# Optimization experiments

Hardware: AMD Instinct MI355X
Metric: run time of the kernel (lower is better)

Reference implementation:

```python
import jax, jax.numpy as jnp
import numpy as np

E = 256  # embedding_dim

def setup_inputs() -> dict:
    key = jax.random.key(0)
    k1, k2, k3 = jax.random.split(key, 3)
    B, P, N, D = 32, 4, 1024, E
    x = jax.random.normal(k1, (B, P, N, D), dtype=jnp.float32)
    W_qkv = jax.random.normal(k2, (D, 1 + 2 * E), dtype=jnp.float32) * (1.0 / np.sqrt(D))
    b_qkv = jnp.zeros((1 + 2 * E,), dtype=jnp.float32)
    W_o = jax.random.normal(k3, (E, E), dtype=jnp.float32) * (1.0 / np.sqrt(E))
    b_o = jnp.zeros((E,), dtype=jnp.float32)
    return {"x": x, "W_qkv": W_qkv, "b_qkv": b_qkv, "W_o": W_o, "b_o": b_o}

def reference(x, W_qkv, b_qkv, W_o, b_o):
    # qkv projection: [B,P,N,D] @ [D,1+2E] -> [B,P,N,1+2E]
    qkv = jnp.einsum('bpnd,de->bpne', x, W_qkv) + b_qkv
    q = qkv[..., :1]                 # [B,P,N,1]
    k = qkv[..., 1:1 + E]            # [B,P,N,E]
    v = jax.nn.relu(qkv[..., 1 + E:])  # [B,P,N,E]
    # softmax over patch axis N (axis=2)
    context_scores = jax.nn.softmax(q, axis=2)
    # context vector: sum over N of k * scores -> [B,P,1,E]
    context_vector = jnp.sum(k * context_scores, axis=2, keepdims=True)
    # broadcast-multiply with relu(v): [B,P,N,E] * [B,P,1,E]
    updated_values = v * context_vector
    # output projection
    out = jnp.einsum('bpnd,de->bpne', updated_values, W_o) + b_o
    return out
```

## Files before the change

### kernel.cpp

```cpp
#include <hip/hip_runtime.h>
#include <hip/hip_bf16.h>

typedef float f32x4 __attribute__((ext_vector_type(4)));
typedef short s16x8 __attribute__((ext_vector_type(8)));
typedef __bf16 bf16x8 __attribute__((ext_vector_type(8)));
typedef unsigned short u16;

#define NSEQ 1024
#define EDIM 256

#define WAITVM(N) asm volatile("s_waitcnt vmcnt(" #N ")" ::: "memory")

__device__ __forceinline__ u16 f2bf(float f){
  union { float f; unsigned u; } v; v.f = f;
  unsigned r = v.u + 0x7FFF + ((v.u >> 16) & 1);
  return (u16)(r >> 16);
}
__device__ __forceinline__ float bf2f(u16 b){
  union { float f; unsigned u; } v; v.u = ((unsigned)b) << 16;
  return v.f;
}

template <typename V>
__device__ __forceinline__ auto mfma_impl(V a, V b, f32x4 c, int)
    -> decltype(__builtin_amdgcn_mfma_f32_16x16x32_bf16(a, b, c, 0, 0, 0)) {
  return __builtin_amdgcn_mfma_f32_16x16x32_bf16(a, b, c, 0, 0, 0);
}
template <typename V>
__device__ __forceinline__ f32x4 mfma_impl(V a, V b, f32x4 c, long){
  bf16x8 ab = __builtin_bit_cast(bf16x8, a);
  bf16x8 bb = __builtin_bit_cast(bf16x8, b);
  return __builtin_amdgcn_mfma_f32_16x16x32_bf16(ab, bb, c, 0, 0, 0);
}
__device__ __forceinline__ f32x4 mfma16(s16x8 a, s16x8 b, f32x4 c){
  return mfma_impl(a, b, c, 0);
}

__device__ __forceinline__ void gload_lds16(const u16* g, u16* l){
  __builtin_amdgcn_global_load_lds((const __attribute__((address_space(1))) void*)g,
                                   (__attribute__((address_space(3))) void*)l, 16, 0, 0);
}

__global__ void k0_prep(const float* __restrict__ Wqkv, const float* __restrict__ Wo,
                        u16* __restrict__ wvf, u16* __restrict__ wof, float* __restrict__ wqc){
  int t = blockIdx.x * 256 + threadIdx.x;
  if (t < 16384){
    int which = t >> 13;
    int slot  = t & 8191;
    int l  = slot & 63;
    int nt = (slot >> 6) & 1;
    int ks = (slot >> 7) & 7;
    int c  = (slot >> 10) & 7;
    int row = ks*32 + 8*(l>>4);
    int col = c*32 + nt*16 + (l&15);
    s16x8 o8;
    if (which == 0){
      for (int j=0;j<8;j++) o8[j] = (short)f2bf(Wqkv[(size_t)(row+j)*513 + 257 + col]);
      *(s16x8*)(wvf + (size_t)slot*8) = o8;
    } else {
      for (int j=0;j<8;j++) o8[j] = (short)f2bf(Wo[(size_t)(row+j)*256 + col]);
      *(s16x8*)(wof + (size_t)slot*8) = o8;
    }
  } else if (t < 16384 + 256){
    int d = t - 16384;
    wqc[d] = Wqkv[(size_t)d*513];
  }
}

__global__ void k1_qfrag(const float* __restrict__ x, const float* __restrict__ wqc,
                         const float* __restrict__ bqkv, u16* __restrict__ xf, float* __restrict__ q){
  int bp = blockIdx.x >> 6, rt = blockIdx.x & 63;
  const float* xt = x + ((size_t)bp*NSEQ + rt*16) * EDIM;
  __shared__ float xl[16][260];
  int tid = threadIdx.x;
  for (int i=0;i<4;i++){
    int idx = tid + i*256;
    float4 vv = ((const float4*)xt)[idx];
    int row = idx >> 6, c4 = idx & 63;
    *(float4*)&xl[row][c4*4] = vv;
  }
  __syncthreads();
  int l = tid & 63, w = tid >> 6;
  int lo = l & 15, hi = l >> 4;
  for (int kk=0;kk<2;kk++){
    int ks = w*2 + kk;
    int k0 = ks*32 + 8*hi;
    s16x8 o8;
    for (int j=0;j<8;j++) o8[j] = (short)f2bf(xl[lo][k0+j]);
    size_t fo = ((((size_t)bp*64 + rt)*8 + ks)*64 + l) * 8;
    *(s16x8*)(xf + fo) = o8;
  }
  int c = l*4;
  float4 wv4 = *(const float4*)(wqc + c);
  float b0 = bqkv[0];
  for (int r=0;r<4;r++){
    int row = w*4 + r;
    float4 xv = *(float4*)&xl[row][c];
    float p = xv.x*wv4.x + xv.y*wv4.y + xv.z*wv4.z + xv.w*wv4.w;
    for (int o=32;o;o>>=1) p += __shfl_down(p, o);
    if (l == 0) q[(size_t)bp*NSEQ + rt*16 + row] = p + b0;
  }
}

__global__ __launch_bounds__(512) void k234(
    const u16* __restrict__ xf, const float* __restrict__ q,
    const float* __restrict__ Wqkv, const float* __restrict__ bqkv,
    float* __restrict__ cv){
  int bp = blockIdx.x;
  int tid = threadIdx.x, l = tid & 63, w = tid >> 6;
  int lo = l & 15, hi = l >> 4;
  __shared__ float sm[1024];
  __shared__ float red[16];
  __shared__ float tl[256];
  __shared__ float cvp[2][256];

  float2 v = ((const float2*)(q + (size_t)bp*NSEQ))[tid];
  float m = fmaxf(v.x, v.y);
  for (int o=32;o;o>>=1) m = fmaxf(m, __shfl_xor(m, o));
  if (l == 0) red[w] = m;
  __syncthreads();
  m = red[0];
#pragma unroll
  for (int i=1;i<8;i++) m = fmaxf(m, red[i]);
  float e0 = expf(v.x - m), e1 = expf(v.y - m);
  float ss = e0 + e1;
  for (int o=32;o;o>>=1) ss += __shfl_xor(ss, o);
  if (l == 0) red[8 + w] = ss;
  __syncthreads();
  float tot = red[8];
#pragma unroll
  for (int i=1;i<8;i++) tot += red[8 + i];
  float inv = 1.0f / tot;
  sm[2*tid]   = e0 * inv;
  sm[2*tid+1] = e1 * inv;
  __syncthreads();

  float acc[8];
#pragma unroll
  for (int j=0;j<8;j++) acc[j] = 0.f;
  const u16* base = xf + (((size_t)bp*64)*8 + w)*512 + (size_t)l*8;
  for (int rt=0; rt<64; rt++){
    s16x8 d8 = *(const s16x8*)(base + (size_t)rt*4096);
    float sv = sm[rt*16 + lo];
#pragma unroll
    for (int j=0;j<8;j++) acc[j] += sv * bf2f((u16)d8[j]);
  }
#pragma unroll
  for (int j=0;j<8;j++)
    for (int mm=1;mm<16;mm<<=1) acc[j] += __shfl_xor(acc[j], mm);
  if (lo == 0){
#pragma unroll
    for (int j=0;j<8;j++) tl[w*32 + 8*hi + j] = acc[j];
  }
  __syncthreads();

  int e = tid & 255, half = tid >> 8;
  float a = 0.f;
  for (int d = half*128; d < half*128 + 128; d++)
    a += tl[d] * Wqkv[(size_t)d*513 + 1 + e];
  cvp[half][e] = a;
  __syncthreads();
  if (tid < 256)
    cv[(size_t)bp*EDIM + tid] = bqkv[1 + tid] + cvp[0][tid] + cvp[1][tid];
}

__global__ __launch_bounds__(256, 2) void k5_main(
    const u16* __restrict__ xf, const u16* __restrict__ wvf, const u16* __restrict__ wof,
    const float* __restrict__ bqkv, const float* __restrict__ bo,
    const float* __restrict__ cv, float* __restrict__ out){
  int bp = blockIdx.x >> 3, rt = blockIdx.x & 7;
  int tid = threadIdx.x, l = tid & 63, w = tid >> 6;
  int lo = l & 15, hi = l >> 4;
  __shared__ u16 WBUF[2][16384];
  __shared__ u16 HB[4][2][16][40];

  auto stage = [&](int chunk, int buf){
    const u16* base = (chunk < 4) ? (wvf + (size_t)chunk*16384)
                                  : (wof + (size_t)(chunk-4)*16384);
    const u16* gsrc = base + (size_t)(w*8)*512 + l*8;
    u16* dst = &WBUF[buf][(size_t)(w*8)*512];
#pragma unroll
    for (int i=0;i<8;i++) gload_lds16(gsrc + i*512, dst + i*512);
  };

  stage(0, 0);

  s16x8 af0[8], af1[8];
  {
    const u16* src0 = xf + ((((size_t)bp*64 + rt*8 + 2*w + 0)*8)*64 + l)*8;
    const u16* src1 = src0 + 4096;
#pragma unroll
    for (int ks=0;ks<8;ks++){
      af0[ks] = *(const s16x8*)(src0 + (size_t)ks*512);
      af1[ks] = *(const s16x8*)(src1 + (size_t)ks*512);
    }
  }
  const float* cvb = cv + (size_t)bp*EDIM;
  float bov[4][4];
#pragma unroll
  for (int cc=0;cc<4;cc++)
#pragma unroll
    for (int qq=0;qq<4;qq++)
      bov[cc][qq] = bo[cc*64 + (qq>>1)*32 + (qq&1)*16 + lo];

  float* ob0 = out + ((size_t)bp*NSEQ + (rt*8 + 2*w + 0)*16) * EDIM;
  float* ob1 = ob0 + 16*EDIM;

  WAITVM(0);
  __builtin_amdgcn_s_barrier();
  __builtin_amdgcn_sched_barrier(0);

  s16x8 hf0[8], hf1[8];

#pragma unroll
  for (int c=0;c<8;c++){
    const int buf = c & 1;
    if (c < 7) stage(c+1, buf^1);

    f32x4 acc0[4], acc1[4];
#pragma unroll
    for (int q=0;q<4;q++){
      acc0[q] = f32x4{0.f,0.f,0.f,0.f};
      acc1[q] = f32x4{0.f,0.f,0.f,0.f};
    }

    __builtin_amdgcn_s_setprio(1);
#pragma unroll
    for (int ks=0;ks<8;ks++){
      s16x8 b[4];
#pragma unroll
      for (int q=0;q<4;q++)
        b[q] = *(const s16x8*)&WBUF[buf][(size_t)(q>>1)*8192 + (size_t)(ks*2+(q&1))*512 + l*8];
#pragma unroll
      for (int q=0;q<4;q++){
        if (c < 4){
          acc0[q] = mfma16(af0[ks], b[q], acc0[q]);
          acc1[q] = mfma16(af1[ks], b[q], acc1[q]);
        } else {
          acc0[q] = mfma16(hf0[ks], b[q], acc0[q]);
          acc1[q] = mfma16(hf1[ks], b[q], acc1[q]);
        }
      }
    }
    __builtin_amdgcn_s_setprio(0);

    if (c < 4){
#pragma unroll
      for (int s=0;s<2;s++){
        int colA = c*64 + s*32 + lo, colB = colA + 16;
        float bvA = bqkv[257 + colA], bvB = bqkv[257 + colB];
        float csA = cvb[colA],        csB = cvb[colB];
#pragma unroll
        for (int r=0;r<4;r++){
          float h00 = acc0[s*2][r]   + bvA, h01 = acc0[s*2+1][r] + bvB;
          float h10 = acc1[s*2][r]   + bvA, h11 = acc1[s*2+1][r] + bvB;
          HB[w][0][hi*4 + r][lo]      = f2bf(h00 > 0.f ? h00*csA : 0.f);
          HB[w][0][hi*4 + r][16 + lo] = f2bf(h01 > 0.f ? h01*csB : 0.f);
          HB[w][1][hi*4 + r][lo]      = f2bf(h10 > 0.f ? h10*csA : 0.f);
          HB[w][1][hi*4 + r][16 + lo] = f2bf(h11 > 0.f ? h11*csB : 0.f);
        }
        hf0[2*c + s] = *(const s16x8*)&HB[w][0][lo][8*hi];
        hf1[2*c + s] = *(const s16x8*)&HB[w][1][lo][8*hi];
      }
    } else {
      int c2 = c - 4;
#pragma unroll
      for (int s=0;s<2;s++){
        int colA = c2*64 + s*32 + lo;
#pragma unroll
        for (int r=0;r<4;r++){
          size_t ro = (size_t)(hi*4 + r)*EDIM;
          ob0[ro + colA]      = acc0[s*2][r]   + bov[c2][s*2];
          ob0[ro + colA + 16] = acc0[s*2+1][r] + bov[c2][s*2+1];
          ob1[ro + colA]      = acc1[s*2][r]   + bov[c2][s*2];
          ob1[ro + colA + 16] = acc1[s*2+1][r] + bov[c2][s*2+1];
        }
      }
    }

    if (c < 7){
      if (c < 4) WAITVM(0); else WAITVM(32);
      __builtin_amdgcn_s_barrier();
      __builtin_amdgcn_sched_barrier(0);
    }
  }
}

extern "C" void kernel_launch(void* const* d_in, const int* in_sizes, int n_in,
                              void* d_out, int out_size, void* d_ws, size_t ws_size,
                              hipStream_t stream){
  const float* x    = (const float*)d_in[0];
  const float* Wqkv = (const float*)d_in[1];
  const float* bqkv = (const float*)d_in[2];
  const float* Wo   = (const float*)d_in[3];
  const float* bo   = (const float*)d_in[4];
  float* out = (float*)d_out;
  char* ws = (char*)d_ws;
  u16*   xf  = (u16*)(ws);
  u16*   wvf = (u16*)(ws + 67108864);
  u16*   wof = (u16*)(ws + 67239936);
  float* q   = (float*)(ws + 67371008);
  float* cvv = (float*)(ws + 69468160);
  float* wqc = (float*)(ws + 69599232);

  hipLaunchKernelGGL(k0_prep,    dim3(65),   dim3(256), 0, stream, Wqkv, Wo, wvf, wof, wqc);
  hipLaunchKernelGGL(k1_qfrag,   dim3(8192), dim3(256), 0, stream, x, wqc, bqkv, xf, q);
  hipLaunchKernelGGL(k234,       dim3(128),  dim3(512), 0, stream, xf, q, Wqkv, bqkv, cvv);
  hipLaunchKernelGGL(k5_main,    dim3(1024), dim3(256), 0, stream, xf, wvf, wof, bqkv, bo, cvv, out);
}
```

Baseline: 125.1 us.

## Compute per-tile online softmax partials in k1 instead of re-reading xf

Kernel k1 now computes, for each 16-row tile, the local max of q, the exp-weighted sum of the fp32 x rows, and the partial denominator, writing small partials instead of the raw q vector. The reduction kernel merges these with a rescaled online-softmax combine, so it no longer re-reads the whole bf16 xf buffer, which removes a large memory pass and a serial loop over 64 tiles. The weighted sum is now taken from fp32 x rather than bf16, and there is an extra partial buffer of 8 MB. k5 also halves its HB shared staging buffer by processing the two row sets sequentially, which may help occupancy but serialises the LDS round trips.

```diff
diff --git a/kernel.cpp b/kernel.cpp
--- a/kernel.cpp
+++ b/kernel.cpp
@@ -68,10 +68,12 @@
 }
 
 __global__ void k1_qfrag(const float* __restrict__ x, const float* __restrict__ wqc,
-                         const float* __restrict__ bqkv, u16* __restrict__ xf, float* __restrict__ q){
+                         const float* __restrict__ bqkv, u16* __restrict__ xf,
+                         float* __restrict__ pm, float* __restrict__ pu){
   int bp = blockIdx.x >> 6, rt = blockIdx.x & 63;
   const float* xt = x + ((size_t)bp*NSEQ + rt*16) * EDIM;
   __shared__ float xl[16][260];
+  __shared__ float qs[16], es[16];
   int tid = threadIdx.x;
   for (int i=0;i<4;i++){
     int idx = tid + i*256;
@@ -98,63 +100,56 @@
     float4 xv = *(float4*)&xl[row][c];
     float p = xv.x*wv4.x + xv.y*wv4.y + xv.z*wv4.z + xv.w*wv4.w;
     for (int o=32;o;o>>=1) p += __shfl_down(p, o);
-    if (l == 0) q[(size_t)bp*NSEQ + rt*16 + row] = p + b0;
-  }
-}
-
-__global__ __launch_bounds__(512) void k234(
-    const u16* __restrict__ xf, const float* __restrict__ q,
+    if (l == 0) qs[row] = p + b0;
+  }
+  __syncthreads();
+  float mb = qs[0];
+#pragma unroll
+  for (int i=1;i<16;i++) mb = fmaxf(mb, qs[i]);
+  if (tid < 16) es[tid] = expf(qs[tid] - mb);
+  __syncthreads();
+  float u = 0.f;
+#pragma unroll
+  for (int r=0;r<16;r++) u += es[r] * xl[r][tid];
+  pu[(((size_t)bp*64 + rt))*256 + tid] = u;
+  if (tid == 0){
+    float zb = 0.f;
+#pragma unroll
+    for (int r=0;r<16;r++) zb += es[r];
+    pm[((size_t)bp*64 + rt)*2 + 0] = mb;
+    pm[((size_t)bp*64 + rt)*2 + 1] = zb;
+  }
+}
+
+__global__ __launch_bounds__(512) void k34(
+    const float* __restrict__ pm, const float* __restrict__ pu,
     const float* __restrict__ Wqkv, const float* __restrict__ bqkv,
     float* __restrict__ cv){
-  int bp = blockIdx.x;
-  int tid = threadIdx.x, l = tid & 63, w = tid >> 6;
-  int lo = l & 15, hi = l >> 4;
-  __shared__ float sm[1024];
-  __shared__ float red[16];
+  int bp = blockIdx.x, tid = threadIdx.x;
+  __shared__ float mzl[128];
+  __shared__ float sf[64];
+  __shared__ float tp2[2][256];
   __shared__ float tl[256];
   __shared__ float cvp[2][256];
-
-  float2 v = ((const float2*)(q + (size_t)bp*NSEQ))[tid];
-  float m = fmaxf(v.x, v.y);
-  for (int o=32;o;o>>=1) m = fmaxf(m, __shfl_xor(m, o));
-  if (l == 0) red[w] = m;
-  __syncthreads();
-  m = red[0];
-#pragma unroll
-  for (int i=1;i<8;i++) m = fmaxf(m, red[i]);
-  float e0 = expf(v.x - m), e1 = expf(v.y - m);
-  float ss = e0 + e1;
-  for (int o=32;o;o>>=1) ss += __shfl_xor(ss, o);
-  if (l == 0) red[8 + w] = ss;
-  __syncthreads();
-  float tot = red[8];
-#pragma unroll
-  for (int i=1;i<8;i++) tot += red[8 + i];
-  float inv = 1.0f / tot;
-  sm[2*tid]   = e0 * inv;
-  sm[2*tid+1] = e1 * inv;
-  __syncthreads();
-
-  float acc[8];
-#pragma unroll
-  for (int j=0;j<8;j++) acc[j] = 0.f;
-  const u16* base = xf + (((size_t)bp*64)*8 + w)*512 + (size_t)l*8;
-  for (int rt=0; rt<64; rt++){
-    s16x8 d8 = *(const s16x8*)(base + (size_t)rt*4096);
-    float sv = sm[rt*16 + lo];
-#pragma unroll
-    for (int j=0;j<8;j++) acc[j] += sv * bf2f((u16)d8[j]);
-  }
-#pragma unroll
-  for (int j=0;j<8;j++)
-    for (int mm=1;mm<16;mm<<=1) acc[j] += __shfl_xor(acc[j], mm);
-  if (lo == 0){
-#pragma unroll
-    for (int j=0;j<8;j++) tl[w*32 + 8*hi + j] = acc[j];
-  }
-  __syncthreads();
-
+  if (tid < 128) mzl[tid] = pm[(size_t)bp*128 + tid];
+  __syncthreads();
+  float M = mzl[0];
+#pragma unroll
+  for (int b=1;b<64;b++) M = fmaxf(M, mzl[2*b]);
+  if (tid < 64) sf[tid] = expf(mzl[2*tid] - M);
+  __syncthreads();
+  float Z = 0.f;
+#pragma unroll
+  for (int b=0;b<64;b++) Z += mzl[2*b+1] * sf[b];
+  float invZ = 1.0f / Z;
   int e = tid & 255, half = tid >> 8;
+  float t = 0.f;
+  for (int b = half*32; b < half*32 + 32; b++)
+    t += pu[((size_t)bp*64 + b)*256 + e] * sf[b];
+  tp2[half][e] = t;
+  __syncthreads();
+  if (tid < 256) tl[tid] = (tp2[0][tid] + tp2[1][tid]) * invZ;
+  __syncthreads();
   float a = 0.f;
   for (int d = half*128; d < half*128 + 128; d++)
     a += tl[d] * Wqkv[(size_t)d*513 + 1 + e];
@@ -172,7 +167,7 @@
   int tid = threadIdx.x, l = tid & 63, w = tid >> 6;
   int lo = l & 15, hi = l >> 4;
   __shared__ u16 WBUF[2][16384];
-  __shared__ u16 HB[4][2][16][40];
+  __shared__ u16 HB[4][16][40];
 
   auto stage = [&](int chunk, int buf){
     const u16* base = (chunk < 4) ? (wvf + (size_t)chunk*16384)
@@ -246,21 +241,22 @@
 
     if (c < 4){
 #pragma unroll
-      for (int s=0;s<2;s++){
-        int colA = c*64 + s*32 + lo, colB = colA + 16;
-        float bvA = bqkv[257 + colA], bvB = bqkv[257 + colB];
-        float csA = cvb[colA],        csB = cvb[colB];
-#pragma unroll
-        for (int r=0;r<4;r++){
-          float h00 = acc0[s*2][r]   + bvA, h01 = acc0[s*2+1][r] + bvB;
-          float h10 = acc1[s*2][r]   + bvA, h11 = acc1[s*2+1][r] + bvB;
-          HB[w][0][hi*4 + r][lo]      = f2bf(h00 > 0.f ? h00*csA : 0.f);
-          HB[w][0][hi*4 + r][16 + lo] = f2bf(h01 > 0.f ? h01*csB : 0.f);
-          HB[w][1][hi*4 + r][lo]      = f2bf(h10 > 0.f ? h10*csA : 0.f);
-          HB[w][1][hi*4 + r][16 + lo] = f2bf(h11 > 0.f ? h11*csB : 0.f);
+      for (int rs=0;rs<2;rs++){
+#pragma unroll
+        for (int s=0;s<2;s++){
+          int colA = c*64 + s*32 + lo, colB = colA + 16;
+          float bvA = bqkv[257 + colA], bvB = bqkv[257 + colB];
+          float csA = cvb[colA],        csB = cvb[colB];
+#pragma unroll
+          for (int r=0;r<4;r++){
+            float hA = (rs ? acc1[s*2][r]   : acc0[s*2][r])   + bvA;
+            float hB = (rs ? acc1[s*2+1][r] : acc0[s*2+1][r]) + bvB;
+            HB[w][hi*4 + r][lo]      = f2bf(hA > 0.f ? hA*csA : 0.f);
+            HB[w][hi*4 + r][16 + lo] = f2bf(hB > 0.f ? hB*csB : 0.f);
+          }
+          if (rs == 0) hf0[2*c + s] = *(const s16x8*)&HB[w][lo][8*hi];
+          else         hf1[2*c + s] = *(const s16x8*)&HB[w][lo][8*hi];
         }
-        hf0[2*c + s] = *(const s16x8*)&HB[w][0][lo][8*hi];
-        hf1[2*c + s] = *(const s16x8*)&HB[w][1][lo][8*hi];
       }
     } else {
       int c2 = c - 4;
@@ -299,12 +295,13 @@
   u16*   xf  = (u16*)(ws);
   u16*   wvf = (u16*)(ws + 67108864);
   u16*   wof = (u16*)(ws + 67239936);
-  float* q   = (float*)(ws + 67371008);
-  float* cvv = (float*)(ws + 69468160);
-  float* wqc = (float*)(ws + 69599232);
-
-  hipLaunchKernelGGL(k0_prep,    dim3(65),   dim3(256), 0, stream, Wqkv, Wo, wvf, wof, wqc);
-  hipLaunchKernelGGL(k1_qfrag,   dim3(8192), dim3(256), 0, stream, x, wqc, bqkv, xf, q);
-  hipLaunchKernelGGL(k234,       dim3(128),  dim3(512), 0, stream, xf, q, Wqkv, bqkv, cvv);
-  hipLaunchKernelGGL(k5_main,    dim3(1024), dim3(256), 0, stream, xf, wvf, wof, bqkv, bo, cvv, out);
-}
+  float* pm  = (float*)(ws + 67371008);
+  float* pu  = (float*)(ws + 67436544);
+  float* cvv = (float*)(ws + 75825152);
+  float* wqc = (float*)(ws + 75956224);
+
+  hipLaunchKernelGGL(k0_prep,  dim3(65),   dim3(256), 0, stream, Wqkv, Wo, wvf, wof, wqc);
+  hipLaunchKernelGGL(k1_qfrag, dim3(8192), dim3(256), 0, stream, x, wqc, bqkv, xf, pm, pu);
+  hipLaunchKernelGGL(k34,      dim3(128),  dim3(512), 0, stream, pm, pu, Wqkv, bqkv, cvv);
+  hipLaunchKernelGGL(k5_main,  dim3(1024), dim3(256), 0, stream, xf, wvf, wof, bqkv, bo, cvv, out);
+}
```

After: 119.0 us. 4.9% less time.
